# Kernel tuning notes

Hardware: AMD Instinct MI355X
Metric: run time of the kernel (lower is better)

Reference implementation:

```python
import jax, jax.numpy as jnp
import numpy as np

G = 32          # num graphs
NPG = 512       # nodes per graph
EPG = 4096      # edges per graph
DN = 128        # node/edge feat dim
DP = 64         # node identifier dim d_p
DE_ID = 64      # type identifier dim d_e
H = 768         # hidden_dim
IN_DIM = DN + 2 * DP + DE_ID  # 320


def setup_inputs() -> dict:
    key = jax.random.key(0)
    ks = jax.random.split(key, 9)
    N = G * NPG
    E = G * EPG
    x = jax.random.normal(ks[0], (N, DN), jnp.float32)
    edge_attr = jax.random.normal(ks[1], (E, DN), jnp.float32)
    P = jax.random.normal(ks[2], (N, DP), jnp.float32)  # ORF node identifiers
    E_V = jax.random.normal(ks[3], (1, DE_ID), jnp.float32) * 0.1
    E_E = jax.random.normal(ks[4], (1, DE_ID), jnp.float32) * 0.1
    W = jax.random.normal(ks[5], (H, IN_DIM), jnp.float32) / np.sqrt(IN_DIM)
    b = jnp.zeros((H,), jnp.float32)
    graph_token = jax.random.normal(ks[6], (1, H), jnp.float32) * 0.1
    # edges stay within their graph and are sorted by graph id
    base = jnp.repeat(jnp.arange(G, dtype=jnp.int32) * NPG, EPG)  # [E]
    src = base + jax.random.randint(ks[7], (E,), 0, NPG, jnp.int32)
    dst = base + jax.random.randint(ks[8], (E,), 0, NPG, jnp.int32)
    edge_index = jnp.stack([src, dst], axis=0)  # [2, E]
    batch = jnp.repeat(jnp.arange(G, dtype=jnp.int32), NPG)  # [N]
    return {
        "x": x, "edge_attr": edge_attr, "P": P,
        "E_V": E_V, "E_E": E_E, "W": W, "b": b, "graph_token": graph_token,
        "edge_index": edge_index, "batch": batch,
        "num_graphs": G, "max_node_num": NPG, "max_edge_num": EPG,
    }


def reference(x, edge_attr, P, E_V, E_E, W, b, graph_token,
              edge_index, batch, num_graphs, max_node_num, max_edge_num):
    N = x.shape[0]
    E = edge_index.shape[1]
    Hd = W.shape[0]
    d_e = E_V.shape[1]

    # node tokens: [x | P | P | E_V] @ W^T + b
    X_v = jnp.concatenate([x, P, P, jnp.broadcast_to(E_V, (N, d_e))], axis=1)
    X_v_proj = X_v @ W.T + b  # [N, H]

    # edge tokens: [edge_attr | P_u | P_v | E_E] @ W^T + b
    P_u = P[edge_index[0]]
    P_v = P[edge_index[1]]
    X_e = jnp.concatenate([edge_attr, P_u, P_v, jnp.broadcast_to(E_E, (E, d_e))], axis=1)
    X_e_proj = X_e @ W.T + b  # [E, H]

    # ragged -> padded packing (replaces per-graph python loop)
    ones_n = jnp.ones((N,), jnp.int32)
    node_num = jax.ops.segment_sum(ones_n, batch, num_segments=num_graphs)  # [G]
    node_ptr = jnp.cumsum(node_num) - node_num  # exclusive prefix sum
    node_pos = jnp.arange(N, dtype=jnp.int32) - node_ptr[batch]  # position within graph

    edge_batch = batch[edge_index[0]]  # [E]
    ones_e = jnp.ones((E,), jnp.int32)
    edge_num = jax.ops.segment_sum(ones_e, edge_batch, num_segments=num_graphs)
    edge_ptr = jnp.cumsum(edge_num) - edge_num
    edge_pos = jnp.arange(E, dtype=jnp.int32) - edge_ptr[edge_batch]

    seq_len = 1 + max_node_num + max_edge_num  # +1 for [graph] token
    tokens = jnp.zeros((num_graphs, seq_len, Hd), X_v_proj.dtype)
    tokens = tokens.at[:, 0, :].set(graph_token[0])
    tokens = tokens.at[batch, 1 + node_pos].set(X_v_proj)
    tokens = tokens.at[edge_batch, 1 + max_node_num + edge_pos].set(X_e_proj)

    attention_masks = jnp.zeros((num_graphs, seq_len), bool)
    attention_masks = attention_masks.at[:, 0].set(True)
    attention_masks = attention_masks.at[batch, 1 + node_pos].set(True)
    attention_masks = attention_masks.at[edge_batch, 1 + max_node_num + edge_pos].set(True)

    return tokens, attention_masks
```

## Files before the change

kernel.cpp:

```cpp
#include <hip/hip_runtime.h>
#include <stdint.h>

#define NG   32
#define NPG  512
#define EPG  4096
#define DN   128
#define DP   64
#define NN   (NG*NPG)
#define NE   (NG*EPG)
#define KD   320
#define HD   768
#define SEQ  (1+NPG+EPG)
#define TOK_ELEMS ((size_t)NG*SEQ*HD)
#define MASK_ELEMS ((size_t)NG*SEQ)

typedef unsigned short u16;
typedef __attribute__((ext_vector_type(8))) __bf16 bf16x8;
typedef __attribute__((ext_vector_type(8))) short  s16x8;
typedef __attribute__((ext_vector_type(4))) float  f32x4;

__device__ __forceinline__ u16 f2bf(float f) {
    uint32_t u = __builtin_bit_cast(uint32_t, f);
    u += 0x7fffu + ((u >> 16) & 1u);
    return (u16)(u >> 16);
}

__device__ __forceinline__ int b_off(int row, int kb) {
    return ((row >> 1) << 7) + ((row & 1) << 6) + (kb ^ (((row >> 1) & 3) << 4));
}

__global__ void ptr_k(const int* __restrict__ batch, const int* __restrict__ eidx,
                      int* __restrict__ nptr, int* __restrict__ eptr) {
    int t = threadIdx.x;
    if (t < NG) {
        int g = t, lo = 0, hi = NN;
        while (lo < hi) { int mid = (lo + hi) >> 1; if (batch[mid] < g) lo = mid + 1; else hi = mid; }
        nptr[g] = lo;
    } else if (t < 2 * NG) {
        int g = t - NG, lo = 0, hi = NE;
        while (lo < hi) { int mid = (lo + hi) >> 1; if (batch[eidx[mid]] < g) lo = mid + 1; else hi = mid; }
        eptr[g] = lo;
    }
}

__global__ void wconv_k(const float* __restrict__ W, u16* __restrict__ Wb) {
    int i = blockIdx.x * 256 + threadIdx.x;
    if (i < KD * HD) Wb[i] = f2bf(W[i]);
}

__global__ void aux_k(const float* __restrict__ gt, float* __restrict__ out) {
    size_t i = (size_t)blockIdx.x * 256 + threadIdx.x;
    if (i < (size_t)NG * HD) {
        int g = (int)(i / HD), c = (int)(i % HD);
        out[(size_t)g * SEQ * HD + c] = gt[c];
    } else {
        size_t m = i - (size_t)NG * HD;
        if (m < MASK_ELEMS) out[TOK_ELEMS + m] = 1.0f;
    }
}

__global__ __launch_bounds__(256, 3)
void gemm_scatter(const float* __restrict__ x,  const float* __restrict__ ea,
                  const float* __restrict__ P,  const float* __restrict__ EV,
                  const float* __restrict__ EEv,const float* __restrict__ bias,
                  const int* __restrict__ eidx, const int* __restrict__ batch,
                  const u16* __restrict__ Wb,   const int* __restrict__ nptr,
                  const int* __restrict__ eptr, float* __restrict__ out)
{
    __shared__ __align__(16) char b_lds[2][8192];
    __shared__ int info_src[128], info_pu[128], info_pv[128], info_orow[128];

    const int tid  = threadIdx.x;
    const int lane = tid & 63;
    const int wid  = tid >> 6;
    const int lrow = lane & 15;
    const int lq   = lane >> 4;

    uint32_t g_off[2], l_off[2];
    #pragma unroll
    for (int i = 0; i < 2; ++i) {
        uint32_t u = (uint32_t)(i * 256 + tid);
        uint32_t row = u >> 3, c = u & 7;
        g_off[i] = row * (KD * 2) + c * 16;
        l_off[i] = ((c >> 2) * 4096u) + (uint32_t)b_off((int)row, (int)((c & 3) * 16));
    }
    const char* WbB = (const char*)Wb;

    const int r0  = blockIdx.x * 128;
    const bool isNode = (r0 < NN);
    const float* feat = isNode ? x  : ea;
    const float* idv  = isNode ? EV : EEv;

    if (tid < 128) {
        int r = r0 + tid;
        if (isNode) {
            int g = batch[r];
            info_src[tid] = r; info_pu[tid] = r; info_pv[tid] = r;
            info_orow[tid] = g * SEQ + 1 + (r - nptr[g]);
        } else {
            int e = r - NN;
            int s = eidx[e], d = eidx[NE + e];
            int g = batch[s];
            info_src[tid] = e; info_pu[tid] = s; info_pv[tid] = d;
            info_orow[tid] = g * SEQ + 1 + NPG + (e - eptr[g]);
        }
    }
    __syncthreads();

    bf16x8 afr[2][10];
    int obase[2][4];
    #pragma unroll
    for (int rb = 0; rb < 2; ++rb) {
        const int arow = wid * 32 + rb * 16 + lrow;
        const int fsrc = info_src[arow];
        const int pu   = info_pu[arow];
        const int pv   = info_pv[arow];
        #pragma unroll
        for (int s = 0; s < 10; ++s) {
            const int kg = s * 32 + lq * 8;
            const float* sp;
            if      (s < 4) sp = feat + (size_t)fsrc * DN + kg;
            else if (s < 6) sp = P + (size_t)pu * DP + (kg - DN);
            else if (s < 8) sp = P + (size_t)pv * DP + (kg - DN - DP);
            else            sp = idv + (kg - DN - 2 * DP);
            f32x4 f0 = *reinterpret_cast<const f32x4*>(sp);
            f32x4 f1 = *reinterpret_cast<const f32x4*>(sp + 4);
            s16x8 v;
            v[0]=(short)f2bf(f0[0]); v[1]=(short)f2bf(f0[1]);
            v[2]=(short)f2bf(f0[2]); v[3]=(short)f2bf(f0[3]);
            v[4]=(short)f2bf(f1[0]); v[5]=(short)f2bf(f1[1]);
            v[6]=(short)f2bf(f1[2]); v[7]=(short)f2bf(f1[3]);
            afr[rb][s] = __builtin_bit_cast(bf16x8, v);
        }
        #pragma unroll
        for (int j = 0; j < 4; ++j)
            obase[rb][j] = info_orow[wid * 32 + rb * 16 + lq * 4 + j] * HD;
    }

    const int roff = b_off(lrow, lq * 16);

    s16x8 pre[2];
    #pragma unroll
    for (int i = 0; i < 2; ++i)
        pre[i] = *reinterpret_cast<const s16x8*>(WbB + g_off[i]);

    int cur = 0;
    int nxt = 1;
    for (int nt = 0; nt < 12; ++nt) {
        const int n0 = nt * 64;
        f32x4 acc[2][4];
        #pragma unroll
        for (int rb = 0; rb < 2; ++rb)
            #pragma unroll
            for (int i = 0; i < 4; ++i) acc[rb][i] = (f32x4)0.f;

        #pragma unroll
        for (int kp = 0; kp < 5; ++kp) {
            cur ^= 1;
            char* bb = &b_lds[0][0] + cur * 8192;
            #pragma unroll
            for (int i = 0; i < 2; ++i)
                *reinterpret_cast<s16x8*>(bb + l_off[i]) = pre[i];
            {
                int tn  = (nxt < 60) ? nxt : 59; ++nxt;
                int ntn = tn / 5, kpn = tn - ntn * 5;
                const char* gb = WbB + (size_t)ntn * (64 * KD * 2) + kpn * 128;
                #pragma unroll
                for (int i = 0; i < 2; ++i)
                    pre[i] = *reinterpret_cast<const s16x8*>(gb + g_off[i]);
            }
            asm volatile("s_waitcnt lgkmcnt(0)" ::: "memory");
            __builtin_amdgcn_sched_barrier(0);
            __builtin_amdgcn_s_barrier();
            #pragma unroll
            for (int kk = 0; kk < 2; ++kk) {
                const int kt = kp * 2 + kk;
                const char* bs = bb + kk * 4096;
                #pragma unroll
                for (int ni = 0; ni < 4; ++ni) {
                    bf16x8 bf = *reinterpret_cast<const bf16x8*>(bs + ni * 1024 + roff);
                    acc[0][ni] = __builtin_amdgcn_mfma_f32_16x16x32_bf16(afr[0][kt], bf, acc[0][ni], 0, 0, 0);
                    acc[1][ni] = __builtin_amdgcn_mfma_f32_16x16x32_bf16(afr[1][kt], bf, acc[1][ni], 0, 0, 0);
                }
            }
        }

        #pragma unroll
        for (int ni = 0; ni < 4; ++ni) {
            float bv = bias[n0 + ni * 16 + lrow];
            #pragma unroll
            for (int rb = 0; rb < 2; ++rb)
                #pragma unroll
                for (int j = 0; j < 4; ++j)
                    out[(size_t)(obase[rb][j] + n0 + ni * 16 + lrow)] =
                        acc[rb][ni][j] + bv;
        }
    }
}

extern "C" void kernel_launch(void* const* d_in, const int* in_sizes, int n_in,
                              void* d_out, int out_size, void* d_ws, size_t ws_size,
                              hipStream_t stream) {
    const float* x    = (const float*)d_in[0];
    const float* ea   = (const float*)d_in[1];
    const float* P    = (const float*)d_in[2];
    const float* EV   = (const float*)d_in[3];
    const float* EEv  = (const float*)d_in[4];
    const float* W    = (const float*)d_in[5];
    const float* bias = (const float*)d_in[6];
    const float* gt   = (const float*)d_in[7];
    const int* eidx   = (const int*)d_in[8];
    const int* batch  = (const int*)d_in[9];

    float* out = (float*)d_out;
    u16* Wb  = (u16*)d_ws;
    int* ints = (int*)((char*)d_ws + (size_t)KD * HD * 2);
    int *nptr = ints, *eptr = ints + 32;

    ptr_k<<<1, 64, 0, stream>>>(batch, eidx, nptr, eptr);
    wconv_k<<<(KD * HD + 255) / 256, 256, 0, stream>>>(W, Wb);
    aux_k<<<(int)(((size_t)NG * HD + MASK_ELEMS + 255) / 256), 256, 0, stream>>>(gt, out);
    gemm_scatter<<<dim3((NN + NE) / 128), 256, 0, stream>>>(
        x, ea, P, EV, EEv, bias, eidx, batch, Wb, nptr, eptr, out);
}
```

Before: 173.2 us.

## Pre-swizzle bf16 weights into MFMA fragment order and load B directly from global

Result: slower. 262.4 us (+51.5%).

```diff
diff --git a/kernel.cpp b/kernel.cpp
--- a/kernel.cpp
+++ b/kernel.cpp
@@ -13,6 +13,7 @@
 #define SEQ  (1+NPG+EPG)
 #define TOK_ELEMS ((size_t)NG*SEQ*HD)
 #define MASK_ELEMS ((size_t)NG*SEQ)
+#define NFRAG (12*10*4*64)
 
 typedef unsigned short u16;
 typedef __attribute__((ext_vector_type(8))) __bf16 bf16x8;
@@ -23,10 +24,6 @@
     uint32_t u = __builtin_bit_cast(uint32_t, f);
     u += 0x7fffu + ((u >> 16) & 1u);
     return (u16)(u >> 16);
-}
-
-__device__ __forceinline__ int b_off(int row, int kb) {
-    return ((row >> 1) << 7) + ((row & 1) << 6) + (kb ^ (((row >> 1) & 3) << 4));
 }
 
 __global__ void ptr_k(const int* __restrict__ batch, const int* __restrict__ eidx,
@@ -43,9 +40,23 @@
     }
 }
 
-__global__ void wconv_k(const float* __restrict__ W, u16* __restrict__ Wb) {
+__global__ void wconv_k(const float* __restrict__ W, u16* __restrict__ Wb2) {
     int i = blockIdx.x * 256 + threadIdx.x;
-    if (i < KD * HD) Wb[i] = f2bf(W[i]);
+    if (i >= NFRAG) return;
+    int nt = i / 2560, rem = i % 2560;
+    int kt = rem / 256, rem2 = rem % 256;
+    int ni = rem2 / 64, lane = rem2 & 63;
+    int row = nt * 64 + ni * 16 + (lane & 15);
+    int k0  = kt * 32 + (lane >> 4) * 8;
+    const float* src = W + (size_t)row * KD + k0;
+    f32x4 f0 = *reinterpret_cast<const f32x4*>(src);
+    f32x4 f1 = *reinterpret_cast<const f32x4*>(src + 4);
+    s16x8 v;
+    v[0]=(short)f2bf(f0[0]); v[1]=(short)f2bf(f0[1]);
+    v[2]=(short)f2bf(f0[2]); v[3]=(short)f2bf(f0[3]);
+    v[4]=(short)f2bf(f1[0]); v[5]=(short)f2bf(f1[1]);
+    v[6]=(short)f2bf(f1[2]); v[7]=(short)f2bf(f1[3]);
+    *reinterpret_cast<s16x8*>(Wb2 + (size_t)i * 8) = v;
 }
 
 __global__ void aux_k(const float* __restrict__ gt, float* __restrict__ out) {
@@ -64,10 +75,9 @@
                   const float* __restrict__ P,  const float* __restrict__ EV,
                   const float* __restrict__ EEv,const float* __restrict__ bias,
                   const int* __restrict__ eidx, const int* __restrict__ batch,
-                  const u16* __restrict__ Wb,   const int* __restrict__ nptr,
+                  const u16* __restrict__ Wb2,  const int* __restrict__ nptr,
                   const int* __restrict__ eptr, float* __restrict__ out)
 {
-    __shared__ __align__(16) char b_lds[2][8192];
     __shared__ int info_src[128], info_pu[128], info_pv[128], info_orow[128];
 
     const int tid  = threadIdx.x;
@@ -75,16 +85,6 @@
     const int wid  = tid >> 6;
     const int lrow = lane & 15;
     const int lq   = lane >> 4;
-
-    uint32_t g_off[2], l_off[2];
-    #pragma unroll
-    for (int i = 0; i < 2; ++i) {
-        uint32_t u = (uint32_t)(i * 256 + tid);
-        uint32_t row = u >> 3, c = u & 7;
-        g_off[i] = row * (KD * 2) + c * 16;
-        l_off[i] = ((c >> 2) * 4096u) + (uint32_t)b_off((int)row, (int)((c & 3) * 16));
-    }
-    const char* WbB = (const char*)Wb;
 
     const int r0  = blockIdx.x * 128;
     const bool isNode = (r0 < NN);
@@ -137,17 +137,11 @@
             obase[rb][j] = info_orow[wid * 32 + rb * 16 + lq * 4 + j] * HD;
     }
 
-    const int roff = b_off(lrow, lq * 16);
-
-    s16x8 pre[2];
-    #pragma unroll
-    for (int i = 0; i < 2; ++i)
-        pre[i] = *reinterpret_cast<const s16x8*>(WbB + g_off[i]);
-
-    int cur = 0;
-    int nxt = 1;
+    const char* pb = (const char*)Wb2 + (size_t)lane * 16;
+
     for (int nt = 0; nt < 12; ++nt) {
         const int n0 = nt * 64;
+        const char* pnt = pb + (size_t)nt * 40960;
         f32x4 acc[2][4];
         #pragma unroll
         for (int rb = 0; rb < 2; ++rb)
@@ -155,33 +149,15 @@
             for (int i = 0; i < 4; ++i) acc[rb][i] = (f32x4)0.f;
 
         #pragma unroll
-        for (int kp = 0; kp < 5; ++kp) {
-            cur ^= 1;
-            char* bb = &b_lds[0][0] + cur * 8192;
-            #pragma unroll
-            for (int i = 0; i < 2; ++i)
-                *reinterpret_cast<s16x8*>(bb + l_off[i]) = pre[i];
-            {
-                int tn  = (nxt < 60) ? nxt : 59; ++nxt;
-                int ntn = tn / 5, kpn = tn - ntn * 5;
-                const char* gb = WbB + (size_t)ntn * (64 * KD * 2) + kpn * 128;
-                #pragma unroll
-                for (int i = 0; i < 2; ++i)
-                    pre[i] = *reinterpret_cast<const s16x8*>(gb + g_off[i]);
-            }
-            asm volatile("s_waitcnt lgkmcnt(0)" ::: "memory");
-            __builtin_amdgcn_sched_barrier(0);
-            __builtin_amdgcn_s_barrier();
-            #pragma unroll
-            for (int kk = 0; kk < 2; ++kk) {
-                const int kt = kp * 2 + kk;
-                const char* bs = bb + kk * 4096;
-                #pragma unroll
-                for (int ni = 0; ni < 4; ++ni) {
-                    bf16x8 bf = *reinterpret_cast<const bf16x8*>(bs + ni * 1024 + roff);
-                    acc[0][ni] = __builtin_amdgcn_mfma_f32_16x16x32_bf16(afr[0][kt], bf, acc[0][ni], 0, 0, 0);
-                    acc[1][ni] = __builtin_amdgcn_mfma_f32_16x16x32_bf16(afr[1][kt], bf, acc[1][ni], 0, 0, 0);
-                }
+        for (int kt = 0; kt < 10; ++kt) {
+            bf16x8 b[4];
+            #pragma unroll
+            for (int ni = 0; ni < 4; ++ni)
+                b[ni] = *reinterpret_cast<const bf16x8*>(pnt + kt * 4096 + ni * 1024);
+            #pragma unroll
+            for (int ni = 0; ni < 4; ++ni) {
+                acc[0][ni] = __builtin_amdgcn_mfma_f32_16x16x32_bf16(afr[0][kt], b[ni], acc[0][ni], 0, 0, 0);
+                acc[1][ni] = __builtin_amdgcn_mfma_f32_16x16x32_bf16(afr[1][kt], b[ni], acc[1][ni], 0, 0, 0);
             }
         }
 
@@ -213,13 +189,13 @@
     const int* batch  = (const int*)d_in[9];
 
     float* out = (float*)d_out;
-    u16* Wb  = (u16*)d_ws;
+    u16* Wb2 = (u16*)d_ws;
     int* ints = (int*)((char*)d_ws + (size_t)KD * HD * 2);
     int *nptr = ints, *eptr = ints + 32;
 
     ptr_k<<<1, 64, 0, stream>>>(batch, eidx, nptr, eptr);
-    wconv_k<<<(KD * HD + 255) / 256, 256, 0, stream>>>(W, Wb);
+    wconv_k<<<(NFRAG + 255) / 256, 256, 0, stream>>>(W, Wb2);
     aux_k<<<(int)(((size_t)NG * HD + MASK_ELEMS + 255) / 256), 256, 0, stream>>>(gt, out);
     gemm_scatter<<<dim3((NN + NE) / 128), 256, 0, stream>>>(
-        x, ea, P, EV, EEv, bias, eidx, batch, Wb, nptr, eptr, out);
-}
+        x, ea, P, EV, EEv, bias, eidx, batch, Wb2, nptr, eptr, out);
+}
```
